# Kernel optimization log

Measured on AMD Instinct MI355X. Metric: run time of the kernel, lower is better.

Reference implementation:

```python
import jax, jax.numpy as jnp
import numpy as np

N_QUBITS = 8
N_LAYERS = 2
FILTERS = 2
K = 2  # kernelsize


def _rx(theta):
    # RX(theta) = [[cos(t/2), -i sin(t/2)], [-i sin(t/2), cos(t/2)]]
    c = jnp.cos(theta / 2)
    s = jnp.sin(theta / 2)
    row0 = jnp.stack([c + 0j, -1j * s])
    row1 = jnp.stack([-1j * s, c + 0j])
    return jnp.stack([row0, row1]).astype(jnp.complex64)


def _apply_1q(state, U, q):
    # state: (2,)*n complex
    state = jnp.moveaxis(state, q, 0)
    state = jnp.tensordot(U, state, axes=[[1], [0]])
    return jnp.moveaxis(state, 0, q)


_CNOT = jnp.array([[1, 0, 0, 0],
                   [0, 1, 0, 0],
                   [0, 0, 0, 1],
                   [0, 0, 1, 0]], dtype=jnp.complex64)


def _apply_cnot(state, c, t):
    n = state.ndim
    state = jnp.moveaxis(state, (c, t), (0, 1))
    shp = state.shape
    state = state.reshape(4, -1)
    state = _CNOT @ state
    state = state.reshape(shp)
    return jnp.moveaxis(state, (0, 1), (c, t))


def _circuit(feat, weights):
    # feat: (K*K,) patch values; weights: (N_LAYERS, N_QUBITS)
    n = N_QUBITS
    state = jnp.zeros((2,) * n, dtype=jnp.complex64).at[(0,) * n].set(1.0)
    # AngleEmbedding (RX) on first K*K wires
    for i in range(K * K):
        state = _apply_1q(state, _rx(feat[i]), i)
    # BasicEntanglerLayers: RX on every wire, then ring of CNOTs
    for l in range(N_LAYERS):
        for q in range(n):
            state = _apply_1q(state, _rx(weights[l, q]), q)
        for q in range(n):
            state = _apply_cnot(state, q, (q + 1) % n)
    probs = jnp.abs(state) ** 2  # (2,)*n real
    z = []
    for q in range(n):
        pq = jnp.moveaxis(probs, q, 0)
        z.append(pq[0].sum() - pq[1].sum())  # expval PauliZ_q
    return jnp.stack(z)  # (n,)


def setup_inputs() -> dict:
    key = jax.random.key(0)
    k1, k2 = jax.random.split(key)
    x = jax.random.normal(k1, (8, 3, 40, 40), dtype=jnp.float32)
    weights = jax.random.normal(k2, (N_LAYERS, N_QUBITS), dtype=jnp.float32)
    return {"x": x, "weights": weights}


def reference(x, weights):
    bs, ch, h, w = x.shape
    h_out = (h - K) // 1 + 1
    w_out = (w - K) // 1 + 1
    # sliding-window patches: (bs, ch, h_out, w_out, K*K)
    patches = jnp.stack(
        [x[:, :, dj:dj + h_out, dk:dk + w_out] for dj in range(K) for dk in range(K)],
        axis=-1,
    )
    feats = patches.reshape(-1, K * K)  # (N, K*K)
    q = jax.vmap(_circuit, in_axes=(0, None))(feats, weights)  # (N, N_QUBITS)
    out = q[:, :FILTERS].reshape(bs, ch, h_out, w_out, FILTERS)
    out = out.mean(axis=1)  # channel-sum then /ch
    out = jnp.moveaxis(out, -1, 1)  # (bs, FILTERS, h_out, w_out)
    return out.astype(jnp.float32)
```

## Files before the change

kernel.cpp:

```cpp
#include <hip/hip_runtime.h>


namespace {

template<int M>
__device__ __forceinline__ void rx_local(float (&sr)[16], float (&si)[16], float c, float s) {
#pragma unroll
    for (int r = 0; r < 16; ++r) {
        if (r & M) continue;
        const int a = r, b = r | M;
        float nra = c*sr[a] + s*si[b], nia = c*si[a] - s*sr[b];
        float nrb = c*sr[b] + s*si[a], nib = c*si[b] - s*sr[a];
        sr[a]=nra; si[a]=nia; sr[b]=nrb; si[b]=nib;
    }
}

__device__ __forceinline__ void rx_lane16(float (&sr)[16], float (&si)[16], float c, float s, int mask) {
#pragma unroll
    for (int r = 0; r < 16; ++r) {
        float orr = __shfl_xor(sr[r], mask, 64);
        float oii = __shfl_xor(si[r], mask, 64);
        sr[r] = c*sr[r] + s*oii;
        si[r] = c*si[r] - s*orr;
    }
}

template<int C, int T>
__device__ __forceinline__ void cnot_ll(float (&sr)[16], float (&si)[16]) {
#pragma unroll
    for (int r = 0; r < 16; ++r) {
        if (!(r & C) || (r & T)) continue;
        const int a = r, b = r ^ T;
        float tr=sr[a], ti=si[a];
        sr[a]=sr[b]; si[a]=si[b];
        sr[b]=tr;    si[b]=ti;
    }
}

__device__ __forceinline__ void entangler(float (&sr)[16], float (&si)[16],
                                          const float* __restrict__ w, int lane) {
    float c, s;
#pragma unroll 1
    for (int l = 0; l < 2; ++l) {
        __sincosf(0.5f*w[l*8+0], &s, &c); rx_local<1>(sr, si, c, s);
        __sincosf(0.5f*w[l*8+1], &s, &c); rx_local<2>(sr, si, c, s);
        __sincosf(0.5f*w[l*8+2], &s, &c); rx_local<4>(sr, si, c, s);
        __sincosf(0.5f*w[l*8+3], &s, &c); rx_local<8>(sr, si, c, s);
        __sincosf(0.5f*w[l*8+4], &s, &c); rx_lane16(sr, si, c, s, 1);
        __sincosf(0.5f*w[l*8+5], &s, &c); rx_lane16(sr, si, c, s, 2);
        __sincosf(0.5f*w[l*8+6], &s, &c); rx_lane16(sr, si, c, s, 4);
        __sincosf(0.5f*w[l*8+7], &s, &c); rx_lane16(sr, si, c, s, 8);

        cnot_ll<1,2>(sr, si);
        cnot_ll<2,4>(sr, si);
        cnot_ll<4,8>(sr, si);
#pragma unroll
        for (int r = 8; r < 16; ++r) {
            sr[r] = __shfl_xor(sr[r], 1, 64);
            si[r] = __shfl_xor(si[r], 1, 64);
        }
#pragma unroll
        for (int qq = 0; qq < 3; ++qq) {
            const int mt = 2 << qq;
            const bool ctrl = (lane >> qq) & 1;
#pragma unroll
            for (int r = 0; r < 16; ++r) {
                float orr = __shfl_xor(sr[r], mt, 64);
                float oii = __shfl_xor(si[r], mt, 64);
                sr[r] = ctrl ? orr : sr[r];
                si[r] = ctrl ? oii : si[r];
            }
        }
        {
            const bool c7 = (lane >> 3) & 1;
#pragma unroll
            for (int r = 0; r < 16; r += 2) {
                float ar = c7 ? sr[r+1] : sr[r];
                float ai = c7 ? si[r+1] : si[r];
                float br = c7 ? sr[r]   : sr[r+1];
                float bi = c7 ? si[r]   : si[r+1];
                sr[r]=ar; si[r]=ai; sr[r+1]=br; si[r+1]=bi;
            }
        }
    }
}

__device__ __forceinline__ int uidx(int n, int g) { return n*16 + g + (n>>4); }

__device__ __forceinline__ void tri_decode(int t, int& rr, int& rp) {
    int r = 0, rem = t;
    while (rem >= 16 - r) { rem -= 16 - r; ++r; }
    rr = r; rp = r + rem;
}

__device__ __forceinline__ int ilv(int bra, int ket) {
    int idx = 0;
#pragma unroll
    for (int k = 0; k < 4; ++k)
        idx |= (((bra>>k)&1) << (2*k+1)) | (((ket>>k)&1) << (2*k));
    return idx;
}

__device__ __forceinline__ void emb_sincos(const float (&f)[12],
                                           float (&vy)[3][4], float (&vz)[3][4]) {
#pragma unroll
    for (int c = 0; c < 3; ++c) {
#pragma unroll
        for (int k = 0; k < 4; ++k) {
            float s, co;
            __sincosf(f[c*4+k], &s, &co);
            vy[c][k] = -s; vz[c][k] = co;
        }
    }
}

}

#define NPIX (8*39*39)
#define BLK  1024
#define PPB  512
#define NBLK ((NPIX + PPB - 1) / PPB)

__global__ __launch_bounds__(1024) void quanv_fused(
    const float* __restrict__ x,
    const float* __restrict__ w,
    float* __restrict__ out)
{
    __shared__ float2 U[16*256 + 16];
    __shared__ float2 XA[2][256];
    __shared__ float2 XB[2][256];
    __shared__ float2 PB[4][2][136];
    __shared__ __align__(16) float Tp[216];

    const int tid  = (int)threadIdx.x;
    const int lane = tid & 63;

    const int half = tid >> 9;
    const int gpix = (int)blockIdx.x * PPB + (tid & 511);
    const int pid  = (gpix < NPIX) ? gpix : (NPIX - 1);
    const int j  = pid % 39;
    const int t2 = pid / 39;
    const int i  = t2 % 39;
    const int b  = t2 / 39;

    float f[12];
#pragma unroll
    for (int c = 0; c < 3; ++c) {
        const float* xp = x + (((b*3 + c)*40) + i)*40 + j;
        f[c*4+0] = xp[0];  f[c*4+1] = xp[1];
        f[c*4+2] = xp[40]; f[c*4+3] = xp[41];
    }

    float vy[3][4], vz[3][4];

    if (tid < 256) {
        const int g = (tid >> 6) * 4 + (lane >> 4);
        float sr[16], si[16];
#pragma unroll
        for (int r = 0; r < 16; ++r) {
            sr[r] = (((lane & 15) == 0) && (r == g)) ? 1.f : 0.f;
            si[r] = 0.f;
        }
        entangler(sr, si, w, lane);
#pragma unroll
        for (int r = 0; r < 16; ++r) {
            const int n = ((lane & 15) << 4) | r;
            U[uidx(n, g)] = make_float2(sr[r], si[r]);
        }
    } else {
        emb_sincos(f, vy, vz);
    }
    __syncthreads();

    if (tid < 544) {
        const int t = tid >> 2, quarter = tid & 3;
        int rr, rp; tri_decode(t, rr, rp);
        float2 a0={0,0}, a1={0,0}, a2={0,0}, a3={0,0};
        const int n0 = quarter * 64;
        for (int n = n0; n < n0 + 64; n += 4) {
#pragma unroll
            for (int cls = 0; cls < 4; ++cls) {
                const float2 ur = U[uidx(n+cls, rr)];
                const float2 up = U[uidx(n+cls, rp)];
                const float cre = ur.x*up.x + ur.y*up.y;
                const float cim = ur.x*up.y - ur.y*up.x;
                if      (cls==0) { a0.x += cre; a0.y += cim; }
                else if (cls==1) { a1.x += cre; a1.y += cim; }
                else if (cls==2) { a2.x += cre; a2.y += cim; }
                else             { a3.x += cre; a3.y += cim; }
            }
        }
        PB[quarter][0][t] = make_float2((a0.x - a1.x) + (a2.x - a3.x),
                                        (a0.y - a1.y) + (a2.y - a3.y));
        PB[quarter][1][t] = make_float2((a0.x + a1.x) - (a2.x + a3.x),
                                        (a0.y + a1.y) - (a2.y + a3.y));
    }
    __syncthreads();

    if (tid < 136) {
        int rr, rp; tri_decode(tid, rr, rp);
        const int idx  = ilv(rr, rp);
        const int idxT = ilv(rp, rr);
#pragma unroll
        for (int q = 0; q < 2; ++q) {
            float2 m = PB[0][q][tid];
            m.x += PB[1][q][tid].x + PB[2][q][tid].x + PB[3][q][tid].x;
            m.y += PB[1][q][tid].y + PB[2][q][tid].y + PB[3][q][tid].y;
            XA[q][idxT] = make_float2(m.x, -m.y);
            XA[q][idx]  = m;
        }
    }
    __syncthreads();

    float2 (*A)[256] = XA;
    float2 (*B)[256] = XB;
    for (int k = 0; k < 4; ++k) {
        if (tid < 128) {
            const int q = tid >> 6, quad = tid & 63;
            const int st = 1 << (2*k);
            const int ml = st - 1;
            const int base = (quad & ml) | ((quad & ~ml) << 2);
            const float2 i00 = A[q][base],      i01 = A[q][base+st];
            const float2 i10 = A[q][base+2*st], i11 = A[q][base+3*st];
            B[q][base]      = make_float2(0.5f*(i00.x+i11.x), 0.5f*(i00.y+i11.y));
            B[q][base+st]   = make_float2(0.5f*(i01.x+i10.x), 0.5f*(i01.y+i10.y));
            B[q][base+2*st] = make_float2(-0.5f*(i01.y-i10.y), 0.5f*(i01.x-i10.x));
            B[q][base+3*st] = make_float2(0.5f*(i00.x-i11.x), 0.5f*(i00.y-i11.y));
        }
        __syncthreads();
        float2 (*t)[256] = A; A = B; B = t;
    }

    if (tid < 162) {
        const int q = tid / 81, u = tid % 81;
        const int i0 = u % 3, i1 = (u/3) % 3, i2 = (u/9) % 3, i3 = u / 27;
        const int p0 = (i0==0)?0:(i0+1);
        const int p1 = (i1==0)?0:(i1+1);
        const int p2 = (i2==0)?0:(i2+1);
        const int p3 = (i3==0)?0:(i3+1);
        const int idx = p0 | (p1<<2) | (p2<<4) | (p3<<6);
        Tp[q*108 + (u/3)*4 + i0] = A[q][idx].x * (1.f/3.f);
    }
    __syncthreads();

    if (gpix < NPIX) {
        if (tid < 256) emb_sincos(f, vy, vz);

        float a3[3] = {0.f, 0.f, 0.f};
#pragma unroll
        for (int i3 = 0; i3 < 3; ++i3) {
            float a2[3] = {0.f, 0.f, 0.f};
#pragma unroll
            for (int i2 = 0; i2 < 3; ++i2) {
                float a1[3] = {0.f, 0.f, 0.f};
#pragma unroll
                for (int i1 = 0; i1 < 3; ++i1) {
                    const float4 tv = *reinterpret_cast<const float4*>(
                        &Tp[half*108 + ((i3*3 + i2)*3 + i1)*4]);
#pragma unroll
                    for (int c = 0; c < 3; ++c) {
                        const float s = fmaf(tv.z, vz[c][0], fmaf(tv.y, vy[c][0], tv.x));
                        if      (i1 == 0) a1[c] += s;
                        else if (i1 == 1) a1[c] = fmaf(s, vy[c][1], a1[c]);
                        else              a1[c] = fmaf(s, vz[c][1], a1[c]);
                    }
                }
#pragma unroll
                for (int c = 0; c < 3; ++c) {
                    if      (i2 == 0) a2[c] += a1[c];
                    else if (i2 == 1) a2[c] = fmaf(a1[c], vy[c][2], a2[c]);
                    else              a2[c] = fmaf(a1[c], vz[c][2], a2[c]);
                }
            }
#pragma unroll
            for (int c = 0; c < 3; ++c) {
                if      (i3 == 0) a3[c] += a2[c];
                else if (i3 == 1) a3[c] = fmaf(a2[c], vy[c][3], a3[c]);
                else              a3[c] = fmaf(a2[c], vz[c][3], a3[c]);
            }
        }

        out[((b*2 + half)*39 + i)*39 + j] = a3[0] + a3[1] + a3[2];
    }
}

extern "C" void kernel_launch(void* const* d_in, const int* in_sizes, int n_in,
                              void* d_out, int out_size, void* d_ws, size_t ws_size,
                              hipStream_t stream) {
    const float* x = (const float*)d_in[0];
    const float* w = (const float*)d_in[1];
    float* out = (float*)d_out;

    quanv_fused<<<NBLK, BLK, 0, stream>>>(x, w, out);
}
```

Baseline: 20.47 us.

## Register-tile the reduced density-matrix contraction and overlap embedding sincos

The per-block U^H·U reduction stage is restructured. Instead of 544 threads each computing one triangular (bra,ket) entry with a decode loop, 256 threads each compute a 1x4 ket tile, loading the bra element once and the kets as float4 vectors, then write a padded PB layout. The full 16x16 matrix is now computed directly, so the conjugate-symmetric fill is gone. The U padding changes to keep vector loads aligned and avoid bank conflicts. The embedding sincos for threads 0-255 is moved into the same phase so it runs concurrently with the contraction rather than after the last sync.

```diff
diff --git a/kernel.cpp b/kernel.cpp
--- a/kernel.cpp
+++ b/kernel.cpp
@@ -85,13 +85,7 @@
     }
 }
 
-__device__ __forceinline__ int uidx(int n, int g) { return n*16 + g + (n>>4); }
-
-__device__ __forceinline__ void tri_decode(int t, int& rr, int& rp) {
-    int r = 0, rem = t;
-    while (rem >= 16 - r) { rem -= 16 - r; ++r; }
-    rr = r; rp = r + rem;
-}
+__device__ __forceinline__ int uidx(int n, int g) { return n*16 + g + ((n>>4)<<1); }
 
 __device__ __forceinline__ int ilv(int bra, int ket) {
     int idx = 0;
@@ -126,10 +120,10 @@
     const float* __restrict__ w,
     float* __restrict__ out)
 {
-    __shared__ float2 U[16*256 + 16];
+    __shared__ __align__(16) float2 U[16*256 + 32];
     __shared__ float2 XA[2][256];
     __shared__ float2 XB[2][256];
-    __shared__ float2 PB[4][2][136];
+    __shared__ float2 PB[4][64][9];
     __shared__ __align__(16) float Tp[216];
 
     const int tid  = (int)threadIdx.x;
@@ -172,43 +166,64 @@
     }
     __syncthreads();
 
-    if (tid < 544) {
-        const int t = tid >> 2, quarter = tid & 3;
-        int rr, rp; tri_decode(t, rr, rp);
-        float2 a0={0,0}, a1={0,0}, a2={0,0}, a3={0,0};
-        const int n0 = quarter * 64;
-        for (int n = n0; n < n0 + 64; n += 4) {
-#pragma unroll
-            for (int cls = 0; cls < 4; ++cls) {
-                const float2 ur = U[uidx(n+cls, rr)];
-                const float2 up = U[uidx(n+cls, rp)];
-                const float cre = ur.x*up.x + ur.y*up.y;
-                const float cim = ur.x*up.y - ur.y*up.x;
-                if      (cls==0) { a0.x += cre; a0.y += cim; }
-                else if (cls==1) { a1.x += cre; a1.y += cim; }
-                else if (cls==2) { a2.x += cre; a2.y += cim; }
-                else             { a3.x += cre; a3.y += cim; }
-            }
-        }
-        PB[quarter][0][t] = make_float2((a0.x - a1.x) + (a2.x - a3.x),
-                                        (a0.y - a1.y) + (a2.y - a3.y));
-        PB[quarter][1][t] = make_float2((a0.x + a1.x) - (a2.x + a3.x),
-                                        (a0.y + a1.y) - (a2.y + a3.y));
+    if (tid < 256) {
+        emb_sincos(f, vy, vz);
+    } else if (tid < 512) {
+        const int bt      = tid - 256;
+        const int tile    = bt & 63;
+        const int quarter = bt >> 6;
+        const int rr  = tile >> 2;
+        const int rp0 = (tile & 3) << 2;
+
+        float2 acc[4][4];
+#pragma unroll
+        for (int cc = 0; cc < 4; ++cc)
+#pragma unroll
+            for (int k = 0; k < 4; ++k) acc[cc][k] = make_float2(0.f, 0.f);
+
+#pragma unroll
+        for (int sub = 0; sub < 4; ++sub) {
+            const int nbase = quarter*64 + sub*16;
+            const float2* Ub = &U[nbase*16 + ((nbase>>4)<<1)];
+            const float2* Ubra = Ub + rr;
+            const float2* Uket = Ub + rp0;
+#pragma unroll
+            for (int ii = 0; ii < 16; ++ii) {
+                const float2 br  = Ubra[ii*16];
+                const float4 k01 = *reinterpret_cast<const float4*>(&Uket[ii*16]);
+                const float4 k23 = *reinterpret_cast<const float4*>(&Uket[ii*16 + 2]);
+                const int cls = ii & 3;
+                acc[cls][0].x += br.x*k01.x + br.y*k01.y;
+                acc[cls][0].y += br.x*k01.y - br.y*k01.x;
+                acc[cls][1].x += br.x*k01.z + br.y*k01.w;
+                acc[cls][1].y += br.x*k01.w - br.y*k01.z;
+                acc[cls][2].x += br.x*k23.x + br.y*k23.y;
+                acc[cls][2].y += br.x*k23.y - br.y*k23.x;
+                acc[cls][3].x += br.x*k23.z + br.y*k23.w;
+                acc[cls][3].y += br.x*k23.w - br.y*k23.z;
+            }
+        }
+#pragma unroll
+        for (int k = 0; k < 4; ++k) {
+            PB[quarter][tile][k*2+0] = make_float2(
+                (acc[0][k].x - acc[1][k].x) + (acc[2][k].x - acc[3][k].x),
+                (acc[0][k].y - acc[1][k].y) + (acc[2][k].y - acc[3][k].y));
+            PB[quarter][tile][k*2+1] = make_float2(
+                (acc[0][k].x + acc[1][k].x) - (acc[2][k].x + acc[3][k].x),
+                (acc[0][k].y + acc[1][k].y) - (acc[2][k].y + acc[3][k].y));
+        }
     }
     __syncthreads();
 
-    if (tid < 136) {
-        int rr, rp; tri_decode(tid, rr, rp);
-        const int idx  = ilv(rr, rp);
-        const int idxT = ilv(rp, rr);
-#pragma unroll
-        for (int q = 0; q < 2; ++q) {
-            float2 m = PB[0][q][tid];
-            m.x += PB[1][q][tid].x + PB[2][q][tid].x + PB[3][q][tid].x;
-            m.y += PB[1][q][tid].y + PB[2][q][tid].y + PB[3][q][tid].y;
-            XA[q][idxT] = make_float2(m.x, -m.y);
-            XA[q][idx]  = m;
-        }
+    if (tid < 512) {
+        const int pair = tid >> 1, q = tid & 1;
+        const int rr = pair >> 4, rp = pair & 15;
+        const int tile = (rr << 2) | (rp >> 2);
+        const int ket  = rp & 3;
+        float2 m = PB[0][tile][ket*2+q];
+        m.x += PB[1][tile][ket*2+q].x + PB[2][tile][ket*2+q].x + PB[3][tile][ket*2+q].x;
+        m.y += PB[1][tile][ket*2+q].y + PB[2][tile][ket*2+q].y + PB[3][tile][ket*2+q].y;
+        XA[q][ilv(rr, rp)] = m;
     }
     __syncthreads();
 
@@ -244,8 +259,6 @@
     __syncthreads();
 
     if (gpix < NPIX) {
-        if (tid < 256) emb_sincos(f, vy, vz);
-
         float a3[3] = {0.f, 0.f, 0.f};
 #pragma unroll
         for (int i3 = 0; i3 < 3; ++i3) {
```

Measured after the change: 28.71 us. +40.3%, slower.
